# Kernel optimization log

Measured on AMD Instinct MI355X. Metric: run time of the kernel, lower is better.

The kernel has to match this reference:

```python
import jax, jax.numpy as jnp
import numpy as np

N_NODES = 50000
N_EDGES = 800000
IN_C, HID_C, OUT_C = 96, 64, 40
ALPHA = 0.2
K = 2
NEG_SLOPE = 0.01  # F.leaky_relu default


def setup_inputs() -> dict:
    key = jax.random.key(0)
    k_x, k_e, k_w0, k_b0, k_w4, k_b4 = jax.random.split(key, 6)
    x = jax.random.normal(k_x, (N_NODES, IN_C), dtype=jnp.float32)
    edge_index = jax.random.randint(k_e, (2, N_EDGES), 0, N_NODES, dtype=jnp.int64)
    # SGConv linear layers (torch.nn.Linear layout: [out, in])
    W0 = jax.random.normal(k_w0, (HID_C, IN_C), dtype=jnp.float32) / np.sqrt(IN_C)
    b0 = jax.random.normal(k_b0, (HID_C,), dtype=jnp.float32) * 0.01
    W4 = jax.random.normal(k_w4, (OUT_C, HID_C), dtype=jnp.float32) / np.sqrt(HID_C)
    b4 = jax.random.normal(k_b4, (OUT_C,), dtype=jnp.float32) * 0.01
    return {"x": x, "edge_index": edge_index, "W0": W0, "b0": b0, "W4": W4, "b4": b4}


def reference(x, edge_index, W0, b0, W4, b4):
    # GCN normalization with self-loops (shared by SGConv and APPNP in PyG):
    # A_hat = A + I, prop(h) = D^{-1/2} A_hat D^{-1/2} h
    n = x.shape[0]
    loops = jnp.arange(n, dtype=edge_index.dtype)
    src = jnp.concatenate([edge_index[0], loops])
    dst = jnp.concatenate([edge_index[1], loops])
    deg = jax.ops.segment_sum(jnp.ones_like(dst, dtype=x.dtype), dst, num_segments=n)
    dinv = jnp.where(deg > 0, jax.lax.rsqrt(deg), 0.0)
    norm = dinv[src] * dinv[dst]  # [E + N]

    def prop(h):
        # gather -> scale -> scatter-add  (irregular memory-bound core op)
        return jax.ops.segment_sum(norm[:, None] * h[src], dst, num_segments=n)

    def sg_prop(h):  # SGConv: K propagation steps, then linear
        for _ in range(K):
            h = prop(h)
        return h

    def appnp(h0):  # APPNP: z_{k+1} = (1-alpha) * prop(z_k) + alpha * h0
        z = h0
        for _ in range(K):
            z = (1.0 - ALPHA) * prop(z) + ALPHA * h0
        return z

    h = sg_prop(x) @ W0.T + b0          # conv0 (SGConv)
    # dropout is identity in eval mode (training=False)
    h = jax.nn.leaky_relu(appnp(h), NEG_SLOPE)   # conv1
    h = jax.nn.leaky_relu(appnp(h), NEG_SLOPE)   # conv2
    h = jax.nn.leaky_relu(appnp(h), NEG_SLOPE)   # conv3
    h = sg_prop(h) @ W4.T + b4          # conv4 (SGConv)
    return jax.nn.log_softmax(h, axis=1)
```

## Files before the change

kernel.cpp:

```cpp
#include <hip/hip_runtime.h>
#include <hip/hip_fp16.h>
#include <math.h>

#define N_NODES 50000
#define N_EDGES 800000
#define IN_C 96
#define HID_C 64
#define OUT_C 40
#define ALPHA 0.2f
#define NEG_SLOPE 0.01f
#define QCAP 131072

typedef _Float16 f16x8 __attribute__((ext_vector_type(8)));
typedef float f32x4 __attribute__((ext_vector_type(4)));

__device__ __forceinline__ int edge_at(const void* ei, int is64, long long pos) {
    return is64 ? (int)((const long long*)ei)[pos] : ((const int*)ei)[pos];
}

__global__ void zero_detect_k(int* deg, int n, int* qtail, const unsigned int* ei, int* flag) {
    int i = blockIdx.x * blockDim.x + threadIdx.x;
    if (i < n) deg[i] = 0;
    if (i < 8) qtail[i] = 0;
    if (i == 0) {
        int is64 = 1;
        for (int j = 1; j < 16; j += 2)
            if (ei[j] != 0u) is64 = 0;
        *flag = is64;
    }
}

__global__ void bucketA_k(const void* ei, const int* flag, int* __restrict__ deg,
                          int* __restrict__ qtail, int2* __restrict__ queue, int E) {
    __shared__ int cnt[8], qb[8];
    int f = *flag;
    int e0 = blockIdx.x * 1024;
    if (threadIdx.x < 8) cnt[threadIdx.x] = 0;
    __syncthreads();
    int s[4], d[4], p[4], r[4];
    #pragma unroll
    for (int k = 0; k < 4; ++k) {
        int e = e0 + threadIdx.x + k * 256;
        if (e < E) {
            d[k] = edge_at(ei, f, (long long)E + e);
            s[k] = edge_at(ei, f, e);
            atomicAdd(&deg[d[k]], 1);
            p[k] = d[k] / (N_NODES / 8);
            if (p[k] > 7) p[k] = 7;
            r[k] = atomicAdd(&cnt[p[k]], 1);
        } else p[k] = -1;
    }
    __syncthreads();
    if (threadIdx.x < 8) qb[threadIdx.x] = atomicAdd(&qtail[threadIdx.x], cnt[threadIdx.x]);
    __syncthreads();
    #pragma unroll
    for (int k = 0; k < 4; ++k) {
        if (p[k] >= 0) {
            int pos = qb[p[k]] + r[k];
            if (pos < QCAP) queue[(size_t)p[k] * QCAP + pos] = make_int2(s[k], d[k]);
        }
    }
}

__global__ void bucketB_k(const int* __restrict__ qtail, const int2* __restrict__ queue,
                          int* __restrict__ cursor, int* __restrict__ csrc) {
    int p = blockIdx.x & 7;
    int j = blockIdx.x >> 3;
    int J = gridDim.x >> 3;
    int n = qtail[p]; if (n > QCAP) n = QCAP;
    const int2* q = queue + (size_t)p * QCAP;
    for (int i = j * blockDim.x + threadIdx.x; i < n; i += J * blockDim.x) {
        int2 e = q[i];
        int pos = atomicAdd(&cursor[e.y], 1);
        csrc[pos] = e.x;
    }
}

__global__ void scan_p1_k(const int* __restrict__ deg, int* __restrict__ part, int n) {
    __shared__ int sm[256];
    int t = threadIdx.x, i = blockIdx.x * 256 + t;
    int v = (i < n) ? deg[i] : 0;
    sm[t] = v;
    __syncthreads();
    for (int off = 1; off < 256; off <<= 1) {
        int u = (t >= off) ? sm[t - off] : 0;
        __syncthreads();
        sm[t] += u;
        __syncthreads();
    }
    if (t == 255) part[blockIdx.x] = sm[255];
}

__global__ void scan_p2_k(int* part, int nb, int* rowptr, int n) {
    __shared__ int sm[256];
    int t = threadIdx.x;
    int v = (t < nb) ? part[t] : 0;
    sm[t] = v;
    __syncthreads();
    for (int off = 1; off < 256; off <<= 1) {
        int u = (t >= off) ? sm[t - off] : 0;
        __syncthreads();
        sm[t] += u;
        __syncthreads();
    }
    if (t < nb) part[t] = sm[t] - v;
    if (t == 255) rowptr[n] = sm[255];
}

__global__ void scan_p3_k(const int* __restrict__ deg, const int* __restrict__ part,
                          int* __restrict__ rowptr, int* __restrict__ cursor,
                          float* __restrict__ dinv, int* __restrict__ bcnt, int n) {
    __shared__ int sm[256];
    __shared__ int h[64];
    int t = threadIdx.x, i = blockIdx.x * 256 + t;
    if (t < 64) h[t] = 0;
    int v = (i < n) ? deg[i] : 0;
    sm[t] = v;
    __syncthreads();
    for (int off = 1; off < 256; off <<= 1) {
        int u = (t >= off) ? sm[t - off] : 0;
        __syncthreads();
        sm[t] += u;
        __syncthreads();
    }
    if (i < n) {
        int excl = sm[t] - v + part[blockIdx.x];
        rowptr[i] = excl;
        cursor[i] = excl;
        dinv[i] = rsqrtf((float)v + 1.0f);
        int dd = v; if (dd > 63) dd = 63;
        atomicAdd(&h[63 - dd], 1);
    }
    __syncthreads();
    if (t < 64) bcnt[blockIdx.x * 64 + t] = h[t];
}

__global__ void bscanA_k(const int* __restrict__ bcnt, int* __restrict__ bbase,
                         int* __restrict__ tot, int nb) {
    __shared__ int sm[256];
    int b = blockIdx.x;
    int t = threadIdx.x;
    int v = (t < nb) ? bcnt[t * 64 + b] : 0;
    sm[t] = v;
    __syncthreads();
    for (int off = 1; off < 256; off <<= 1) {
        int u = (t >= off) ? sm[t - off] : 0;
        __syncthreads();
        sm[t] += u;
        __syncthreads();
    }
    if (t < nb) bbase[t * 64 + b] = sm[t] - v;
    if (t == 255) tot[b] = sm[255];
}

__global__ void perm_k(const int* __restrict__ deg, const int* __restrict__ bbase,
                       const int* __restrict__ tot, int* __restrict__ perm, int n) {
    __shared__ int h[64], bs[64];
    int t = threadIdx.x, i = blockIdx.x * 256 + t;
    if (t < 64) { h[t] = 0; bs[t] = tot[t]; }
    __syncthreads();
    if (t == 0) {
        int run = 0;
        for (int k = 0; k < 64; ++k) { int v = bs[k]; bs[k] = run; run += v; }
    }
    __syncthreads();
    if (i < n) {
        int d = deg[i]; if (d > 63) d = 63;
        int b = 63 - d;
        int rank = atomicAdd(&h[b], 1);
        perm[bs[b] + bbase[blockIdx.x * 64 + b] + rank] = i;
    }
}

__device__ __forceinline__ void add8(float* acc, float4 v, float w) {
    const __half2* hp = (const __half2*)&v;
    #pragma unroll
    for (int j = 0; j < 4; ++j) {
        float2 f = __half22float2(hp[j]);
        acc[2 * j] += w * f.x;
        acc[2 * j + 1] += w * f.y;
    }
}

template <bool COMBINE, bool LEAKY, bool BIAS>
__global__ void __launch_bounds__(256) prop64_k(
        const int* __restrict__ perm,
        const int* __restrict__ rowptr, const int* __restrict__ csrc,
        const float* __restrict__ dinv,
        const __half* __restrict__ in, const __half* __restrict__ h0,
        const float* __restrict__ bias,
        __half* __restrict__ out, int N) {
    int g = blockIdx.x * (blockDim.x >> 3) + (threadIdx.x >> 3);
    int ci = threadIdx.x & 7;
    if (g >= N) return;
    int node = perm[g];
    const float4* in8 = (const float4*)in;
    float acc[8];
    {
        float4 r = in8[node * 8 + ci];
        const __half2* hp = (const __half2*)&r;
        #pragma unroll
        for (int j = 0; j < 4; ++j) {
            float2 f = __half22float2(hp[j]);
            acc[2 * j] = f.x;
            acc[2 * j + 1] = f.y;
        }
    }
    int r0 = rowptr[node], r1 = rowptr[node + 1];
    int i = r0;
    for (; i + 3 < r1; i += 4) {
        int s0 = csrc[i], s1 = csrc[i + 1], s2 = csrc[i + 2], s3 = csrc[i + 3];
        float4 v0 = in8[s0 * 8 + ci];
        float4 v1 = in8[s1 * 8 + ci];
        float4 v2 = in8[s2 * 8 + ci];
        float4 v3 = in8[s3 * 8 + ci];
        add8(acc, v0, 1.0f);
        add8(acc, v1, 1.0f);
        add8(acc, v2, 1.0f);
        add8(acc, v3, 1.0f);
    }
    for (; i < r1; ++i) {
        float4 v0 = in8[csrc[i] * 8 + ci];
        add8(acc, v0, 1.0f);
    }
    float di = dinv[node];
    float sc = di * di;
    float v[8];
    #pragma unroll
    for (int j = 0; j < 8; ++j) v[j] = sc * acc[j];
    if (BIAS) {
        float4 b0v = ((const float4*)bias)[2 * ci];
        float4 b1v = ((const float4*)bias)[2 * ci + 1];
        v[0] += di * b0v.x; v[1] += di * b0v.y; v[2] += di * b0v.z; v[3] += di * b0v.w;
        v[4] += di * b1v.x; v[5] += di * b1v.y; v[6] += di * b1v.z; v[7] += di * b1v.w;
    }
    if (COMBINE) {
        float4 r = ((const float4*)h0)[node * 8 + ci];
        const __half2* hp = (const __half2*)&r;
        #pragma unroll
        for (int j = 0; j < 4; ++j) {
            float2 f = __half22float2(hp[j]);
            v[2 * j]     = (1.0f - ALPHA) * v[2 * j]     + ALPHA * f.x;
            v[2 * j + 1] = (1.0f - ALPHA) * v[2 * j + 1] + ALPHA * f.y;
        }
    }
    if (LEAKY) {
        #pragma unroll
        for (int j = 0; j < 8; ++j) v[j] = v[j] > 0.0f ? v[j] : NEG_SLOPE * v[j];
    }
    float4 o;
    __half2* op = (__half2*)&o;
    #pragma unroll
    for (int j = 0; j < 4; ++j)
        op[j] = __float22half2_rn(make_float2(v[2 * j], v[2 * j + 1]));
    ((float4*)out)[node * 8 + ci] = o;
}

__global__ void prop40_k(const int* __restrict__ perm,
                         const int* __restrict__ rowptr, const int* __restrict__ csrc,
                         const float* __restrict__ dinv,
                         const __half* __restrict__ in, __half* __restrict__ out, int N) {
    constexpr int CP = OUT_C / 2;
    int hw = blockIdx.x * (blockDim.x >> 5) + (threadIdx.x >> 5);
    int ci = threadIdx.x & 31;
    if (hw >= N) return;
    int node = perm[hw];
    bool act = ci < CP;
    const __half2* in2 = (const __half2*)in;
    float2 acc = make_float2(0.0f, 0.0f);
    if (act) {
        acc = __half22float2(in2[(long long)node * CP + ci]);
    }
    int r0 = rowptr[node], r1 = rowptr[node + 1];
    int i = r0;
    for (; i + 3 < r1; i += 4) {
        int s0 = csrc[i], s1 = csrc[i + 1], s2 = csrc[i + 2], s3 = csrc[i + 3];
        if (act) {
            float2 v0 = __half22float2(in2[(long long)s0 * CP + ci]);
            float2 v1 = __half22float2(in2[(long long)s1 * CP + ci]);
            float2 v2 = __half22float2(in2[(long long)s2 * CP + ci]);
            float2 v3 = __half22float2(in2[(long long)s3 * CP + ci]);
            acc.x += (v0.x + v1.x) + (v2.x + v3.x);
            acc.y += (v0.y + v1.y) + (v2.y + v3.y);
        }
    }
    for (; i < r1; ++i) {
        int s0 = csrc[i];
        if (act) {
            float2 v0 = __half22float2(in2[(long long)s0 * CP + ci]);
            acc.x += v0.x; acc.y += v0.y;
        }
    }
    if (act) {
        float di = dinv[node];
        float sc = di * di;
        ((__half2*)out)[(long long)node * CP + ci] =
            __float22half2_rn(make_float2(sc * acc.x, sc * acc.y));
    }
}

__global__ void prop40_softmax_k(const int* __restrict__ perm,
                                 const int* __restrict__ rowptr, const int* __restrict__ csrc,
                                 const float* __restrict__ dinv,
                                 const __half* __restrict__ in, const float* __restrict__ bias,
                                 float* __restrict__ out, int N) {
    constexpr int CP = OUT_C / 2;
    int hw = blockIdx.x * (blockDim.x >> 5) + (threadIdx.x >> 5);
    int ci = threadIdx.x & 31;
    if (hw >= N) return;
    int node = perm[hw];
    bool act = ci < CP;
    const __half2* in2 = (const __half2*)in;
    float2 acc = make_float2(0.0f, 0.0f);
    if (act) {
        acc = __half22float2(in2[(long long)node * CP + ci]);
    }
    int r0 = rowptr[node], r1 = rowptr[node + 1];
    int i = r0;
    for (; i + 3 < r1; i += 4) {
        int s0 = csrc[i], s1 = csrc[i + 1], s2 = csrc[i + 2], s3 = csrc[i + 3];
        if (act) {
            float2 v0 = __half22float2(in2[(long long)s0 * CP + ci]);
            float2 v1 = __half22float2(in2[(long long)s1 * CP + ci]);
            float2 v2 = __half22float2(in2[(long long)s2 * CP + ci]);
            float2 v3 = __half22float2(in2[(long long)s3 * CP + ci]);
            acc.x += (v0.x + v1.x) + (v2.x + v3.x);
            acc.y += (v0.y + v1.y) + (v2.y + v3.y);
        }
    }
    for (; i < r1; ++i) {
        int s0 = csrc[i];
        if (act) {
            float2 v0 = __half22float2(in2[(long long)s0 * CP + ci]);
            acc.x += v0.x; acc.y += v0.y;
        }
    }
    float di = dinv[node];
    float2 v = make_float2(-INFINITY, -INFINITY);
    if (act) {
        v.x = di * acc.x + bias[2 * ci];
        v.y = di * acc.y + bias[2 * ci + 1];
    }
    float m = fmaxf(v.x, v.y);
    #pragma unroll
    for (int off = 16; off >= 1; off >>= 1) m = fmaxf(m, __shfl_xor(m, off));
    float e = act ? (expf(v.x - m) + expf(v.y - m)) : 0.0f;
    #pragma unroll
    for (int off = 16; off >= 1; off >>= 1) e += __shfl_xor(e, off);
    float ls = m + logf(e);
    if (act)
        ((float2*)out)[(long long)node * CP + ci] = make_float2(v.x - ls, v.y - ls);
}

template <int O, int K, bool FP32IN, bool SCALE>
__global__ void __launch_bounds__(256) mfma_lin_k(const void* __restrict__ in_,
                                                  const float* __restrict__ W,
                                                  const float* __restrict__ dinv,
                                                  __half* __restrict__ out, int Mtiles) {
    constexpr int P2 = 52;
    __shared__ __half2 wsh[O * P2];
    for (int idx = threadIdx.x; idx < O * (K / 2); idx += 256) {
        int o = idx / (K / 2), kk = idx - o * (K / 2);
        float2 w2 = ((const float2*)W)[o * (K / 2) + kk];
        wsh[o * P2 + kk] = __floats2half2_rn(w2.x, w2.y);
    }
    __syncthreads();
    int wave = (blockIdx.x * 256 + threadIdx.x) >> 6;
    if (wave >= Mtiles) return;
    int lane = threadIdx.x & 63;
    int lm = lane & 15, q = lane >> 4;
    long long m0 = (long long)wave * 16;
    constexpr int NT = (O + 15) / 16;
    f32x4 acc[NT];
    #pragma unroll
    for (int j = 0; j < NT; ++j) acc[j] = (f32x4){0.f, 0.f, 0.f, 0.f};
    const __half* wsp = (const __half*)wsh;
    #pragma unroll
    for (int k0 = 0; k0 < K; k0 += 32) {
        f16x8 a;
        if (FP32IN) {
            const float* xr = (const float*)in_ + (m0 + lm) * K + k0 + q * 8;
            float4 x0 = ((const float4*)xr)[0];
            float4 x1 = ((const float4*)xr)[1];
            a = (f16x8){(_Float16)x0.x, (_Float16)x0.y, (_Float16)x0.z, (_Float16)x0.w,
                        (_Float16)x1.x, (_Float16)x1.y, (_Float16)x1.z, (_Float16)x1.w};
        } else {
            const __half* xr = (const __half*)in_ + (m0 + lm) * K + k0 + q * 8;
            a = *(const f16x8*)xr;
        }
        #pragma unroll
        for (int j = 0; j < NT; ++j) {
            f16x8 b = *(const f16x8*)(wsp + (16 * j + lm) * (2 * P2) + k0 + q * 8);
            acc[j] = __builtin_amdgcn_mfma_f32_16x16x32_f16(a, b, acc[j], 0, 0, 0);
        }
    }
    #pragma unroll
    for (int r = 0; r < 4; ++r) {
        long long m = m0 + q * 4 + r;
        float sc = SCALE ? dinv[m] : 1.0f;
        #pragma unroll
        for (int j = 0; j < NT; ++j) {
            int col = 16 * j + lm;
            if (col < O) out[m * O + col] = __float2half(acc[j][r] * sc);
        }
    }
}

static inline int cdiv(long long a, long long b) { return (int)((a + b - 1) / b); }
static inline size_t align256(size_t x) { return (x + 255) & ~(size_t)255; }

extern "C" void kernel_launch(void* const* d_in, const int* in_sizes, int n_in,
                              void* d_out, int out_size, void* d_ws, size_t ws_size,
                              hipStream_t stream) {
    const float* x  = (const float*)d_in[0];
    const void*  ei = d_in[1];
    const float* W0 = (const float*)d_in[2];
    const float* b0 = (const float*)d_in[3];
    const float* W4 = (const float*)d_in[4];
    const float* b4 = (const float*)d_in[5];
    float* out = (float*)d_out;

    const int N = N_NODES, E = N_EDGES;
    const int NB = cdiv(N, 256);
    char* ws = (char*)d_ws;
    int*    flag   = (int*)ws;     ws += 256;
    int*    deg    = (int*)ws;     ws += align256((size_t)N * 4);
    int*    rowptr = (int*)ws;     ws += align256((size_t)(N + 1) * 4);
    int*    cursor = (int*)ws;     ws += align256((size_t)N * 4);
    int*    part   = (int*)ws;     ws += align256(256 * 4);
    int*    bcnt   = (int*)ws;     ws += align256((size_t)NB * 64 * 4);
    int*    bbase  = (int*)ws;     ws += align256((size_t)NB * 64 * 4);
    int*    tot    = (int*)ws;     ws += align256(64 * 4);
    int*    qtail  = (int*)ws;     ws += align256(8 * 4);
    int*    perm   = (int*)ws;     ws += align256((size_t)N * 4);
    float*  dinv   = (float*)ws;   ws += align256((size_t)N * 4);
    int*    csrc   = (int*)ws;     ws += align256((size_t)E * 4);
    int2*   queue  = (int2*)ws;    ws += align256((size_t)8 * QCAP * 8);
    __half* bufA   = (__half*)ws;  ws += align256((size_t)N * HID_C * 2);
    __half* bufB   = (__half*)ws;  ws += align256((size_t)N * HID_C * 2);
    __half* bufC   = (__half*)ws;  ws += align256((size_t)N * HID_C * 2);

    const int T = 256;
    const int MT = N / 16;
    const int LB = cdiv(MT, 4);
    const int P64B = cdiv(N, T / 8);
    const int P40B = cdiv(N, T / 32);

    zero_detect_k<<<cdiv(N, T), T, 0, stream>>>(deg, N, qtail, (const unsigned int*)ei, flag);
    bucketA_k<<<cdiv(E, 1024), T, 0, stream>>>(ei, flag, deg, qtail, queue, E);
    scan_p1_k<<<NB, 256, 0, stream>>>(deg, part, N);
    scan_p2_k<<<1, 256, 0, stream>>>(part, NB, rowptr, N);
    scan_p3_k<<<NB, 256, 0, stream>>>(deg, part, rowptr, cursor, dinv, bcnt, N);
    bscanA_k<<<64, 256, 0, stream>>>(bcnt, bbase, tot, NB);
    perm_k<<<NB, 256, 0, stream>>>(deg, bbase, tot, perm, N);
    bucketB_k<<<8 * 64, T, 0, stream>>>(qtail, queue, cursor, csrc);

    mfma_lin_k<HID_C, IN_C, true, true><<<LB, 256, 0, stream>>>(x, W0, dinv, bufA, MT);
    prop64_k<false, false, false><<<P64B, T, 0, stream>>>(
        perm, rowptr, csrc, dinv, bufA, nullptr, nullptr, bufB, N);
    prop64_k<false, false, true><<<P64B, T, 0, stream>>>(
        perm, rowptr, csrc, dinv, bufB, nullptr, b0, bufC, N);

    for (int r = 0; r < 3; ++r) {
        prop64_k<true, false, false><<<P64B, T, 0, stream>>>(
            perm, rowptr, csrc, dinv, bufC, bufC, nullptr, bufB, N);
        prop64_k<true, true, false><<<P64B, T, 0, stream>>>(
            perm, rowptr, csrc, dinv, bufB, bufC, nullptr, bufC, N);
    }

    mfma_lin_k<OUT_C, HID_C, false, false><<<LB, 256, 0, stream>>>(bufC, W4, dinv, bufA, MT);
    prop40_k<<<P40B, T, 0, stream>>>(perm, rowptr, csrc, dinv, bufA, bufB, N);
    prop40_softmax_k<<<P40B, T, 0, stream>>>(perm, rowptr, csrc, dinv, bufB, b4, out, N);
}
```

Measured before the change: 343.9 us.

## Split 64-channel features into two 32-channel planes and widen 40-channel propagation

Stores the 64-channel hidden features as two planes of 32 halves each. Each propagation block handles one plane, with 4 threads per node instead of 8, so each gathered row is 64 bytes and the per-pass working set is halved for better cache locality. The MFMA linear kernels gain plane-aware input and output indexing. The 40-channel propagation and softmax kernels switch from 32 lanes of half2 to 8 lanes of float4 with 5 active, cutting wasted lanes. The cost is two blocks per node and duplicate index and rowptr reads per plane.

```diff
diff --git a/kernel.cpp b/kernel.cpp
--- a/kernel.cpp
+++ b/kernel.cpp
@@ -10,6 +10,9 @@
 #define ALPHA 0.2f
 #define NEG_SLOPE 0.01f
 #define QCAP 131072
+
+#define PLANE_H ((size_t)N_NODES * 32)
+#define PLANE_F4 ((size_t)N_NODES * 4)
 
 typedef _Float16 f16x8 __attribute__((ext_vector_type(8)));
 typedef float f32x4 __attribute__((ext_vector_type(4)));
@@ -183,21 +186,94 @@
 }
 
 template <bool COMBINE, bool LEAKY, bool BIAS>
-__global__ void __launch_bounds__(256) prop64_k(
+__global__ void __launch_bounds__(256) prop32_k(
         const int* __restrict__ perm,
         const int* __restrict__ rowptr, const int* __restrict__ csrc,
         const float* __restrict__ dinv,
         const __half* __restrict__ in, const __half* __restrict__ h0,
         const float* __restrict__ bias,
         __half* __restrict__ out, int N) {
+    int half = blockIdx.x & 1;
+    int g = (blockIdx.x >> 1) * (blockDim.x >> 2) + (threadIdx.x >> 2);
+    int ci = threadIdx.x & 3;
+    if (g >= N) return;
+    int node = perm[g];
+    const float4* in4 = (const float4*)in + (size_t)half * PLANE_F4;
+    float acc[8];
+    {
+        float4 r = in4[(size_t)node * 4 + ci];
+        const __half2* hp = (const __half2*)&r;
+        #pragma unroll
+        for (int j = 0; j < 4; ++j) {
+            float2 f = __half22float2(hp[j]);
+            acc[2 * j] = f.x;
+            acc[2 * j + 1] = f.y;
+        }
+    }
+    int r0 = rowptr[node], r1 = rowptr[node + 1];
+    int i = r0;
+    for (; i + 3 < r1; i += 4) {
+        int s0 = csrc[i], s1 = csrc[i + 1], s2 = csrc[i + 2], s3 = csrc[i + 3];
+        float4 v0 = in4[(size_t)s0 * 4 + ci];
+        float4 v1 = in4[(size_t)s1 * 4 + ci];
+        float4 v2 = in4[(size_t)s2 * 4 + ci];
+        float4 v3 = in4[(size_t)s3 * 4 + ci];
+        add8(acc, v0, 1.0f);
+        add8(acc, v1, 1.0f);
+        add8(acc, v2, 1.0f);
+        add8(acc, v3, 1.0f);
+    }
+    for (; i < r1; ++i) {
+        float4 v0 = in4[(size_t)csrc[i] * 4 + ci];
+        add8(acc, v0, 1.0f);
+    }
+    float di = dinv[node];
+    float sc = di * di;
+    float v[8];
+    #pragma unroll
+    for (int j = 0; j < 8; ++j) v[j] = sc * acc[j];
+    if (BIAS) {
+        float4 b0v = ((const float4*)bias)[half * 8 + 2 * ci];
+        float4 b1v = ((const float4*)bias)[half * 8 + 2 * ci + 1];
+        v[0] += di * b0v.x; v[1] += di * b0v.y; v[2] += di * b0v.z; v[3] += di * b0v.w;
+        v[4] += di * b1v.x; v[5] += di * b1v.y; v[6] += di * b1v.z; v[7] += di * b1v.w;
+    }
+    if (COMBINE) {
+        float4 r = ((const float4*)h0 + (size_t)half * PLANE_F4)[(size_t)node * 4 + ci];
+        const __half2* hp = (const __half2*)&r;
+        #pragma unroll
+        for (int j = 0; j < 4; ++j) {
+            float2 f = __half22float2(hp[j]);
+            v[2 * j]     = (1.0f - ALPHA) * v[2 * j]     + ALPHA * f.x;
+            v[2 * j + 1] = (1.0f - ALPHA) * v[2 * j + 1] + ALPHA * f.y;
+        }
+    }
+    if (LEAKY) {
+        #pragma unroll
+        for (int j = 0; j < 8; ++j) v[j] = v[j] > 0.0f ? v[j] : NEG_SLOPE * v[j];
+    }
+    float4 o;
+    __half2* op = (__half2*)&o;
+    #pragma unroll
+    for (int j = 0; j < 4; ++j)
+        op[j] = __float22half2_rn(make_float2(v[2 * j], v[2 * j + 1]));
+    ((float4*)out + (size_t)half * PLANE_F4)[(size_t)node * 4 + ci] = o;
+}
+
+__global__ void __launch_bounds__(256) prop40_k(
+        const int* __restrict__ perm,
+        const int* __restrict__ rowptr, const int* __restrict__ csrc,
+        const float* __restrict__ dinv,
+        const __half* __restrict__ in, __half* __restrict__ out, int N) {
     int g = blockIdx.x * (blockDim.x >> 3) + (threadIdx.x >> 3);
     int ci = threadIdx.x & 7;
     if (g >= N) return;
     int node = perm[g];
-    const float4* in8 = (const float4*)in;
-    float acc[8];
-    {
-        float4 r = in8[node * 8 + ci];
+    bool act = ci < 5;
+    const float4* in4 = (const float4*)in;
+    float acc[8] = {0.f, 0.f, 0.f, 0.f, 0.f, 0.f, 0.f, 0.f};
+    if (act) {
+        float4 r = in4[(size_t)node * 5 + ci];
         const __half2* hp = (const __half2*)&r;
         #pragma unroll
         for (int j = 0; j < 4; ++j) {
@@ -205,154 +281,121 @@
             acc[2 * j] = f.x;
             acc[2 * j + 1] = f.y;
         }
-    }
-    int r0 = rowptr[node], r1 = rowptr[node + 1];
-    int i = r0;
-    for (; i + 3 < r1; i += 4) {
-        int s0 = csrc[i], s1 = csrc[i + 1], s2 = csrc[i + 2], s3 = csrc[i + 3];
-        float4 v0 = in8[s0 * 8 + ci];
-        float4 v1 = in8[s1 * 8 + ci];
-        float4 v2 = in8[s2 * 8 + ci];
-        float4 v3 = in8[s3 * 8 + ci];
-        add8(acc, v0, 1.0f);
-        add8(acc, v1, 1.0f);
-        add8(acc, v2, 1.0f);
-        add8(acc, v3, 1.0f);
-    }
-    for (; i < r1; ++i) {
-        float4 v0 = in8[csrc[i] * 8 + ci];
-        add8(acc, v0, 1.0f);
-    }
-    float di = dinv[node];
-    float sc = di * di;
-    float v[8];
-    #pragma unroll
-    for (int j = 0; j < 8; ++j) v[j] = sc * acc[j];
-    if (BIAS) {
-        float4 b0v = ((const float4*)bias)[2 * ci];
-        float4 b1v = ((const float4*)bias)[2 * ci + 1];
-        v[0] += di * b0v.x; v[1] += di * b0v.y; v[2] += di * b0v.z; v[3] += di * b0v.w;
-        v[4] += di * b1v.x; v[5] += di * b1v.y; v[6] += di * b1v.z; v[7] += di * b1v.w;
-    }
-    if (COMBINE) {
-        float4 r = ((const float4*)h0)[node * 8 + ci];
-        const __half2* hp = (const __half2*)&r;
-        #pragma unroll
-        for (int j = 0; j < 4; ++j) {
-            float2 f = __half22float2(hp[j]);
-            v[2 * j]     = (1.0f - ALPHA) * v[2 * j]     + ALPHA * f.x;
-            v[2 * j + 1] = (1.0f - ALPHA) * v[2 * j + 1] + ALPHA * f.y;
-        }
-    }
-    if (LEAKY) {
-        #pragma unroll
-        for (int j = 0; j < 8; ++j) v[j] = v[j] > 0.0f ? v[j] : NEG_SLOPE * v[j];
-    }
-    float4 o;
-    __half2* op = (__half2*)&o;
-    #pragma unroll
-    for (int j = 0; j < 4; ++j)
-        op[j] = __float22half2_rn(make_float2(v[2 * j], v[2 * j + 1]));
-    ((float4*)out)[node * 8 + ci] = o;
-}
-
-__global__ void prop40_k(const int* __restrict__ perm,
-                         const int* __restrict__ rowptr, const int* __restrict__ csrc,
-                         const float* __restrict__ dinv,
-                         const __half* __restrict__ in, __half* __restrict__ out, int N) {
-    constexpr int CP = OUT_C / 2;
-    int hw = blockIdx.x * (blockDim.x >> 5) + (threadIdx.x >> 5);
-    int ci = threadIdx.x & 31;
-    if (hw >= N) return;
-    int node = perm[hw];
-    bool act = ci < CP;
-    const __half2* in2 = (const __half2*)in;
-    float2 acc = make_float2(0.0f, 0.0f);
-    if (act) {
-        acc = __half22float2(in2[(long long)node * CP + ci]);
     }
     int r0 = rowptr[node], r1 = rowptr[node + 1];
     int i = r0;
     for (; i + 3 < r1; i += 4) {
         int s0 = csrc[i], s1 = csrc[i + 1], s2 = csrc[i + 2], s3 = csrc[i + 3];
         if (act) {
-            float2 v0 = __half22float2(in2[(long long)s0 * CP + ci]);
-            float2 v1 = __half22float2(in2[(long long)s1 * CP + ci]);
-            float2 v2 = __half22float2(in2[(long long)s2 * CP + ci]);
-            float2 v3 = __half22float2(in2[(long long)s3 * CP + ci]);
-            acc.x += (v0.x + v1.x) + (v2.x + v3.x);
-            acc.y += (v0.y + v1.y) + (v2.y + v3.y);
+            float4 v0 = in4[(size_t)s0 * 5 + ci];
+            float4 v1 = in4[(size_t)s1 * 5 + ci];
+            float4 v2 = in4[(size_t)s2 * 5 + ci];
+            float4 v3 = in4[(size_t)s3 * 5 + ci];
+            add8(acc, v0, 1.0f);
+            add8(acc, v1, 1.0f);
+            add8(acc, v2, 1.0f);
+            add8(acc, v3, 1.0f);
         }
     }
     for (; i < r1; ++i) {
         int s0 = csrc[i];
         if (act) {
-            float2 v0 = __half22float2(in2[(long long)s0 * CP + ci]);
-            acc.x += v0.x; acc.y += v0.y;
+            float4 v0 = in4[(size_t)s0 * 5 + ci];
+            add8(acc, v0, 1.0f);
         }
     }
     if (act) {
         float di = dinv[node];
         float sc = di * di;
-        ((__half2*)out)[(long long)node * CP + ci] =
-            __float22half2_rn(make_float2(sc * acc.x, sc * acc.y));
-    }
-}
-
-__global__ void prop40_softmax_k(const int* __restrict__ perm,
-                                 const int* __restrict__ rowptr, const int* __restrict__ csrc,
-                                 const float* __restrict__ dinv,
-                                 const __half* __restrict__ in, const float* __restrict__ bias,
-                                 float* __restrict__ out, int N) {
-    constexpr int CP = OUT_C / 2;
-    int hw = blockIdx.x * (blockDim.x >> 5) + (threadIdx.x >> 5);
-    int ci = threadIdx.x & 31;
-    if (hw >= N) return;
-    int node = perm[hw];
-    bool act = ci < CP;
-    const __half2* in2 = (const __half2*)in;
-    float2 acc = make_float2(0.0f, 0.0f);
+        float4 o;
+        __half2* op = (__half2*)&o;
+        #pragma unroll
+        for (int j = 0; j < 4; ++j)
+            op[j] = __float22half2_rn(make_float2(sc * acc[2 * j], sc * acc[2 * j + 1]));
+        ((float4*)out)[(size_t)node * 5 + ci] = o;
+    }
+}
+
+__global__ void __launch_bounds__(256) prop40_softmax_k(
+        const int* __restrict__ perm,
+        const int* __restrict__ rowptr, const int* __restrict__ csrc,
+        const float* __restrict__ dinv,
+        const __half* __restrict__ in, const float* __restrict__ bias,
+        float* __restrict__ out, int N) {
+    int g = blockIdx.x * (blockDim.x >> 3) + (threadIdx.x >> 3);
+    int ci = threadIdx.x & 7;
+    if (g >= N) return;
+    int node = perm[g];
+    bool act = ci < 5;
+    const float4* in4 = (const float4*)in;
+    float acc[8] = {0.f, 0.f, 0.f, 0.f, 0.f, 0.f, 0.f, 0.f};
     if (act) {
-        acc = __half22float2(in2[(long long)node * CP + ci]);
+        float4 r = in4[(size_t)node * 5 + ci];
+        const __half2* hp = (const __half2*)&r;
+        #pragma unroll
+        for (int j = 0; j < 4; ++j) {
+            float2 f = __half22float2(hp[j]);
+            acc[2 * j] = f.x;
+            acc[2 * j + 1] = f.y;
+        }
     }
     int r0 = rowptr[node], r1 = rowptr[node + 1];
     int i = r0;
     for (; i + 3 < r1; i += 4) {
         int s0 = csrc[i], s1 = csrc[i + 1], s2 = csrc[i + 2], s3 = csrc[i + 3];
         if (act) {
-            float2 v0 = __half22float2(in2[(long long)s0 * CP + ci]);
-            float2 v1 = __half22float2(in2[(long long)s1 * CP + ci]);
-            float2 v2 = __half22float2(in2[(long long)s2 * CP + ci]);
-            float2 v3 = __half22float2(in2[(long long)s3 * CP + ci]);
-            acc.x += (v0.x + v1.x) + (v2.x + v3.x);
-            acc.y += (v0.y + v1.y) + (v2.y + v3.y);
+            float4 v0 = in4[(size_t)s0 * 5 + ci];
+            float4 v1 = in4[(size_t)s1 * 5 + ci];
+            float4 v2 = in4[(size_t)s2 * 5 + ci];
+            float4 v3 = in4[(size_t)s3 * 5 + ci];
+            add8(acc, v0, 1.0f);
+            add8(acc, v1, 1.0f);
+            add8(acc, v2, 1.0f);
+            add8(acc, v3, 1.0f);
         }
     }
     for (; i < r1; ++i) {
         int s0 = csrc[i];
         if (act) {
-            float2 v0 = __half22float2(in2[(long long)s0 * CP + ci]);
-            acc.x += v0.x; acc.y += v0.y;
+            float4 v0 = in4[(size_t)s0 * 5 + ci];
+            add8(acc, v0, 1.0f);
         }
     }
     float di = dinv[node];
-    float2 v = make_float2(-INFINITY, -INFINITY);
+    float v[8];
     if (act) {
-        v.x = di * acc.x + bias[2 * ci];
-        v.y = di * acc.y + bias[2 * ci + 1];
-    }
-    float m = fmaxf(v.x, v.y);
-    #pragma unroll
-    for (int off = 16; off >= 1; off >>= 1) m = fmaxf(m, __shfl_xor(m, off));
-    float e = act ? (expf(v.x - m) + expf(v.y - m)) : 0.0f;
-    #pragma unroll
-    for (int off = 16; off >= 1; off >>= 1) e += __shfl_xor(e, off);
+        float4 b0v = ((const float4*)bias)[2 * ci];
+        float4 b1v = ((const float4*)bias)[2 * ci + 1];
+        v[0] = di * acc[0] + b0v.x; v[1] = di * acc[1] + b0v.y;
+        v[2] = di * acc[2] + b0v.z; v[3] = di * acc[3] + b0v.w;
+        v[4] = di * acc[4] + b1v.x; v[5] = di * acc[5] + b1v.y;
+        v[6] = di * acc[6] + b1v.z; v[7] = di * acc[7] + b1v.w;
+    } else {
+        #pragma unroll
+        for (int j = 0; j < 8; ++j) v[j] = -INFINITY;
+    }
+    float m = v[0];
+    #pragma unroll
+    for (int j = 1; j < 8; ++j) m = fmaxf(m, v[j]);
+    #pragma unroll
+    for (int off = 4; off >= 1; off >>= 1) m = fmaxf(m, __shfl_xor(m, off));
+    float e = 0.0f;
+    if (act) {
+        #pragma unroll
+        for (int j = 0; j < 8; ++j) e += expf(v[j] - m);
+    }
+    #pragma unroll
+    for (int off = 4; off >= 1; off >>= 1) e += __shfl_xor(e, off);
     float ls = m + logf(e);
-    if (act)
-        ((float2*)out)[(long long)node * CP + ci] = make_float2(v.x - ls, v.y - ls);
-}
-
-template <int O, int K, bool FP32IN, bool SCALE>
+    if (act) {
+        float4 o0 = make_float4(v[0] - ls, v[1] - ls, v[2] - ls, v[3] - ls);
+        float4 o1 = make_float4(v[4] - ls, v[5] - ls, v[6] - ls, v[7] - ls);
+        ((float4*)out)[(size_t)node * 10 + 2 * ci] = o0;
+        ((float4*)out)[(size_t)node * 10 + 2 * ci + 1] = o1;
+    }
+}
+
+template <int O, int K, bool FP32IN, bool SCALE, bool PIN, bool POUT>
 __global__ void __launch_bounds__(256) mfma_lin_k(const void* __restrict__ in_,
                                                   const float* __restrict__ W,
                                                   const float* __restrict__ dinv,
@@ -384,6 +427,10 @@
             float4 x1 = ((const float4*)xr)[1];
             a = (f16x8){(_Float16)x0.x, (_Float16)x0.y, (_Float16)x0.z, (_Float16)x0.w,
                         (_Float16)x1.x, (_Float16)x1.y, (_Float16)x1.z, (_Float16)x1.w};
+        } else if (PIN) {
+            const __half* xr = (const __half*)in_ + (size_t)(k0 >> 5) * PLANE_H
+                               + (m0 + lm) * 32 + q * 8;
+            a = *(const f16x8*)xr;
         } else {
             const __half* xr = (const __half*)in_ + (m0 + lm) * K + k0 + q * 8;
             a = *(const f16x8*)xr;
@@ -401,7 +448,12 @@
         #pragma unroll
         for (int j = 0; j < NT; ++j) {
             int col = 16 * j + lm;
-            if (col < O) out[m * O + col] = __float2half(acc[j][r] * sc);
+            if (POUT) {
+                out[(size_t)(col >> 5) * PLANE_H + m * 32 + (col & 31)] =
+                    __float2half(acc[j][r] * sc);
+            } else if (col < O) {
+                out[m * O + col] = __float2half(acc[j][r] * sc);
+            }
         }
     }
 }
@@ -443,8 +495,8 @@
     const int T = 256;
     const int MT = N / 16;
     const int LB = cdiv(MT, 4);
-    const int P64B = cdiv(N, T / 8);
-    const int P40B = cdiv(N, T / 32);
+    const int P32B = 2 * cdiv(N, T / 4);
+    const int P40B = cdiv(N, T / 8);
 
     zero_detect_k<<<cdiv(N, T), T, 0, stream>>>(deg, N, qtail, (const unsigned int*)ei, flag);
     bucketA_k<<<cdiv(E, 1024), T, 0, stream>>>(ei, flag, deg, qtail, queue, E);
@@ -455,20 +507,22 @@
     perm_k<<<NB, 256, 0, stream>>>(deg, bbase, tot, perm, N);
     bucketB_k<<<8 * 64, T, 0, stream>>>(qtail, queue, cursor, csrc);
 
-    mfma_lin_k<HID_C, IN_C, true, true><<<LB, 256, 0, stream>>>(x, W0, dinv, bufA, MT);
-    prop64_k<false, false, false><<<P64B, T, 0, stream>>>(
+    mfma_lin_k<HID_C, IN_C, true, true, false, true><<<LB, 256, 0, stream>>>(
+        x, W0, dinv, bufA, MT);
+    prop32_k<false, false, false><<<P32B, T, 0, stream>>>(
         perm, rowptr, csrc, dinv, bufA, nullptr, nullptr, bufB, N);
-    prop64_k<false, false, true><<<P64B, T, 0, stream>>>(
+    prop32_k<false, false, true><<<P32B, T, 0, stream>>>(
         perm, rowptr, csrc, dinv, bufB, nullptr, b0, bufC, N);
 
     for (int r = 0; r < 3; ++r) {
-        prop64_k<true, false, false><<<P64B, T, 0, stream>>>(
+        prop32_k<true, false, false><<<P32B, T, 0, stream>>>(
             perm, rowptr, csrc, dinv, bufC, bufC, nullptr, bufB, N);
-        prop64_k<true, true, false><<<P64B, T, 0, stream>>>(
+        prop32_k<true, true, false><<<P32B, T, 0, stream>>>(
             perm, rowptr, csrc, dinv, bufB, bufC, nullptr, bufC, N);
     }
 
-    mfma_lin_k<OUT_C, HID_C, false, false><<<LB, 256, 0, stream>>>(bufC, W4, dinv, bufA, MT);
+    mfma_lin_k<OUT_C, HID_C, false, false, true, false><<<LB, 256, 0, stream>>>(
+        bufC, W4, dinv, bufA, MT);
     prop40_k<<<P40B, T, 0, stream>>>(perm, rowptr, csrc, dinv, bufA, bufB, N);
     prop40_softmax_k<<<P40B, T, 0, stream>>>(perm, rowptr, csrc, dinv, bufB, b4, out, N);
 }
```

Result: slower. 368.3 us (+7.1%).
